# Performance work log

Measured on AMD Instinct MI355X. Metric: run time of the kernel, lower is better.

Reference implementation:

```python
import jax, jax.numpy as jnp
import numpy as np

# ---- static configuration (mirrors EarthSpecificBlock/EarthAttention3D) ----
WS = (2, 6, 12)                 # window_size (Z, H, W)
DIM = 192
HEADS = 6
DEPTH = 2
B, Z, H, W = 1, 8, 91, 180      # token grid entering the layer
PAD_H = (WS[1] - H % WS[1]) % WS[1]   # 5
PAD_W = (WS[2] - W % WS[2]) % WS[2]   # 0
HP, WP = H + PAD_H, W + PAD_W         # 96, 180
TOK = WS[0] * WS[1] * WS[2]           # 144 tokens per window
NZ, NH, NW = Z // WS[0], HP // WS[1], WP // WS[2]   # 4, 16, 15
TYPE_W = NZ * NH                      # 64 window types (Z x lat)
BIAS_ROWS = (2 * WS[2] - 1) * WS[1] * WS[1] * WS[0] * WS[0]  # 3312


def _construct_index():
    """Position index into the earth-specific bias table (EarthAttention3D._construct_index)."""
    zi = np.arange(WS[0]); zj = -np.arange(WS[0]) * WS[0]
    hi = np.arange(WS[1]); hj = -np.arange(WS[1]) * WS[1]
    w = np.arange(WS[2])
    c1 = np.stack(np.meshgrid(zi, hi, w, indexing='ij')).reshape(3, -1)
    c2 = np.stack(np.meshgrid(zj, hj, w, indexing='ij')).reshape(3, -1)
    coords = (c1[:, :, None] - c2[:, None, :]).transpose(1, 2, 0)
    coords[:, :, 2] += WS[2] - 1
    coords[:, :, 1] *= 2 * WS[2] - 1
    coords[:, :, 0] *= (2 * WS[2] - 1) * WS[1] * WS[1]
    return coords.sum(-1).reshape(-1)   # (TOK*TOK,)


def _gen_mask():
    """Shifted-window attention mask (gen_mask), shape (1, NW, TYPE_W, 1, TOK, TOK)."""
    m = np.zeros((1, Z, HP, WP, 1), np.float32)
    zs = (slice(0, -WS[0]), slice(-WS[0], -WS[0] // 2), slice(-WS[0] // 2, None))
    hs = (slice(0, -WS[1]), slice(-WS[1], -WS[1] // 2), slice(-WS[1] // 2, None))
    cnt = 0
    for zsl in zs:
        for hsl in hs:
            m[:, zsl, hsl, :, :] = cnt
            cnt += 1
    mw = m.reshape(1, NZ, WS[0], NH, WS[1], NW, WS[2], 1).transpose(0, 1, 3, 5, 2, 4, 6, 7)
    mw = mw.reshape(1, NZ, NH, NW, TOK)
    am = mw[:, :, :, :, None, :] - mw[:, :, :, :, :, None]
    am = np.where(am != 0, np.float32(-100.0), np.float32(0.0))
    return am.transpose(0, 3, 1, 2, 4, 5).reshape(1, NW, TYPE_W, 1, TOK, TOK)


POS_IDX = jnp.asarray(_construct_index())
MASK = jnp.asarray(_gen_mask())


def _ln(x, g, b):
    m = x.mean(-1, keepdims=True)
    v = ((x - m) ** 2).mean(-1, keepdims=True)
    return (x - m) * jax.lax.rsqrt(v + 1e-5) * g + b


def _block(x, qkv_w, qkv_b, proj_w, proj_b, bias_tab, g1, b1, g2, b2, w1, bm1, w2, bm2, roll):
    shortcut = x
    x = jnp.pad(x, ((0, 0), (0, 0), (0, PAD_H), (0, PAD_W), (0, 0)))
    if roll:
        x = jnp.roll(x, (-(WS[0] // 2), -(WS[1] // 2), -(WS[2] // 2)), axis=(1, 2, 3))
    # window partition: (B, NW, TYPE_W, TOK, C)
    xw = x.reshape(B, NZ, WS[0], NH, WS[1], NW, WS[2], DIM).transpose(0, 5, 1, 3, 2, 4, 6, 7)
    xw = xw.reshape(B, NW, TYPE_W, TOK, DIM)
    dh = DIM // HEADS
    qkv = (xw @ qkv_w + qkv_b).reshape(B, NW, TYPE_W, TOK, 3, HEADS, dh)
    qkv = qkv.transpose(4, 0, 1, 2, 5, 3, 6)   # (3, B, NW, TYPE_W, HEADS, TOK, dh)
    q, k, v = qkv[0], qkv[1], qkv[2]
    q = q * (dh ** -0.5)
    attn = jnp.einsum('bwphid,bwphjd->bwphij', q, k)
    bias = bias_tab[POS_IDX].reshape(TOK, TOK, TYPE_W, HEADS).transpose(2, 3, 0, 1)
    attn = attn + bias
    if roll:
        attn = attn + MASK
    attn = jax.nn.softmax(attn, axis=-1)
    out = jnp.einsum('bwphij,bwphjd->bwphid', attn, v)
    out = out.transpose(0, 1, 2, 4, 3, 5).reshape(B, NW, TYPE_W, TOK, DIM)
    out = out @ proj_w + proj_b
    # window merge back to (B, Z, HP, WP, C)
    x = out.reshape(B, NW, NZ, NH, WS[0], WS[1], WS[2], DIM).transpose(0, 2, 4, 3, 5, 1, 6, 7)
    x = x.reshape(B, Z, HP, WP, DIM)
    if roll:
        x = jnp.roll(x, (WS[0] // 2, WS[1] // 2, WS[2] // 2), axis=(1, 2, 3))
    x = x[:, :, :H, :W]
    x = shortcut + _ln(x, g1, b1)           # post-norm residual, as in source
    h = jax.nn.gelu(x @ w1 + bm1, approximate=False)
    h = h @ w2 + bm2
    return x + _ln(h, g2, b2)


def setup_inputs() -> dict:
    key = jax.random.key(0)
    ks = jax.random.split(key, 8)
    s = 0.02
    return {
        'x': jax.random.normal(ks[0], (B, Z, H, W, DIM), jnp.float32),
        'qkv_w': jax.random.normal(ks[1], (DEPTH, DIM, 3 * DIM), jnp.float32) * s,
        'qkv_b': jnp.zeros((DEPTH, 3 * DIM), jnp.float32),
        'proj_w': jax.random.normal(ks[2], (DEPTH, DIM, DIM), jnp.float32) * s,
        'proj_b': jnp.zeros((DEPTH, DIM), jnp.float32),
        'bias_tab': jax.random.normal(ks[3], (DEPTH, BIAS_ROWS, TYPE_W, HEADS), jnp.float32) * s,
        'norm1_g': jnp.ones((DEPTH, DIM), jnp.float32),
        'norm1_b': jnp.zeros((DEPTH, DIM), jnp.float32),
        'norm2_g': jnp.ones((DEPTH, DIM), jnp.float32),
        'norm2_b': jnp.zeros((DEPTH, DIM), jnp.float32),
        'mlp_w1': jax.random.normal(ks[4], (DEPTH, DIM, 4 * DIM), jnp.float32) * s,
        'mlp_b1': jnp.zeros((DEPTH, 4 * DIM), jnp.float32),
        'mlp_w2': jax.random.normal(ks[5], (DEPTH, 4 * DIM, DIM), jnp.float32) * s,
        'mlp_b2': jnp.zeros((DEPTH, DIM), jnp.float32),
    }


def reference(x, qkv_w, qkv_b, proj_w, proj_b, bias_tab, norm1_g, norm1_b,
              norm2_g, norm2_b, mlp_w1, mlp_b1, mlp_w2, mlp_b2):
    for i in range(DEPTH):
        x = _block(x, qkv_w[i], qkv_b[i], proj_w[i], proj_b[i], bias_tab[i],
                   norm1_g[i], norm1_b[i], norm2_g[i], norm2_b[i],
                   mlp_w1[i], mlp_b1[i], mlp_w2[i], mlp_b2[i], roll=(i % 2 == 1))
    return x
```

## Files before the change

kernel.cpp:

```cpp
#include <hip/hip_runtime.h>
#include <math.h>

#define NTOK   131040
#define NTOKW  138240

typedef __attribute__((ext_vector_type(8))) short bf16x8;
typedef __attribute__((ext_vector_type(8))) unsigned short u16x8;
typedef __attribute__((ext_vector_type(4))) float f32x4;
typedef __attribute__((ext_vector_type(2))) float f32x2;

__device__ __forceinline__ float b2f(unsigned short u){
  union { unsigned u; float f; } v; v.u = ((unsigned)u) << 16; return v.f;
}
__device__ __forceinline__ unsigned short f2b(float f){
  union { float f; unsigned u; } v; v.f = f;
  unsigned r = v.u + 0x7FFFu + ((v.u >> 16) & 1u);
  return (unsigned short)(r >> 16);
}
__device__ __forceinline__ float gelu_fast(float x){
  float t = 0.79788456080286536f * (x + 0.044715f * x * x * x);
  float e = __expf(2.0f * t);
  float th = 1.0f - 2.0f * __builtin_amdgcn_rcpf(e + 1.0f);
  return 0.5f * x * (1.0f + th);
}
__device__ __forceinline__ unsigned pk_bf16(float lo, float hi){
  unsigned r;
  asm("v_cvt_pk_bf16_f32 %0, %1, %2" : "=v"(r) : "v"(lo), "v"(hi));
  return r;
}
__device__ __forceinline__ void lds_barrier(){
  asm volatile("s_waitcnt lgkmcnt(0)" ::: "memory");
  __builtin_amdgcn_sched_barrier(0);
  __builtin_amdgcn_s_barrier();
  __builtin_amdgcn_sched_barrier(0);
}

__global__ __launch_bounds__(256) void transp(const float* __restrict__ src,
                                              unsigned short* __restrict__ dst,
                                              int K, int N){
  int i = blockIdx.x*256 + threadIdx.x;
  if (i < K*N){
    int n = i / K, k = i % K;
    dst[i] = f2b(src[(size_t)k*N + n]);
  }
}

__global__ __launch_bounds__(256) void bias_pre(
    const float* __restrict__ btab,
    unsigned short* __restrict__ bw,
    int roll)
{
  int gid = blockIdx.x*256 + threadIdx.x;
  int pair = gid / 20736;
  int rem  = gid % 20736;
  int i = rem / 144, j = rem % 144;
  int tw = pair / 6, head = pair % 6;
  int ia = i/72, ib = (i%72)/12, ic = i%12;
  int ja = j/72, jb = (j%72)/12, jc = j%12;
  int idx = (ia + 2*ja)*828 + (ib + 6*jb)*23 + (ic - jc + 11);
  float v = btab[(size_t)idx*384 + tw*6 + head];
  if (roll){
    int nz = tw >> 4, nh = tw & 15;
    int zi = nz*2+ia, hi = nh*6+ib, zj = nz*2+ja, hj = nh*6+jb;
    int ri = 3*((zi<6)?0:((zi<7)?1:2)) + ((hi<90)?0:((hi<93)?1:2));
    int rj = 3*((zj<6)?0:((zj<7)?1:2)) + ((hj<90)?0:((hj<93)?1:2));
    if (ri != rj) v -= 100.0f;
  }
  bw[gid] = f2b(v);
}

__global__ __launch_bounds__(256) void gather_win(const float* __restrict__ x,
                                                  unsigned short* __restrict__ xw,
                                                  int roll){
  int gid = blockIdx.x*256 + threadIdx.x;
  int row = gid / 24;
  int dp  = gid % 24;
  int tok = row % 144;
  int wt  = row / 144;
  int tw  = wt & 63;
  int w   = wt >> 6;
  int nz = tw >> 4, nh = tw & 15;
  int wz = tok / 72; int rem = tok % 72; int wh = rem / 12; int ww = rem % 12;
  int z = nz*2 + wz, h = nh*6 + wh, wc = w*12 + ww;
  if (roll){ z = (z+1)&7; h = (h+3)%96; wc = (wc+6)%180; }
  int d0 = dp*8;
  u16x8 o;
  if (h < 91){
    const float* s = x + ((size_t)((z*91 + h)*180 + wc))*192 + d0;
    #pragma unroll
    for (int i=0;i<8;i++) o[i] = f2b(s[i]);
  } else {
    #pragma unroll
    for (int i=0;i<8;i++) o[i] = 0;
  }
  *(u16x8*)(xw + (size_t)row*192 + d0) = o;
}

__global__ __launch_bounds__(512) void gemm_k192(
    const unsigned short* __restrict__ A,
    const unsigned short* __restrict__ Bt,
    const float* __restrict__ bias,
    unsigned short* __restrict__ C,
    int N)
{
  __shared__ unsigned short Bst[192][200];
  int m0 = blockIdx.x * 128;
  int n0 = blockIdx.y * 192;
  int t = threadIdx.x;
  int lane = t & 63, w = t >> 6;
  int wm = w >> 2, wn = w & 3;
  int lg = lane >> 4, lr = lane & 15;

  #pragma unroll
  for (int i=0;i<9;i++){
    int idx = t + i*512;
    int r = idx / 24, c = (idx % 24)*8;
    *(u16x8*)&Bst[r][c] = *(const u16x8*)(Bt + (size_t)(n0 + r)*192 + c);
  }
  __syncthreads();

  const unsigned short* aRow = A + (size_t)(m0 + wm*64 + lr)*192 + lg*8;

  f32x4 acc[4][3];
  #pragma unroll
  for (int a=0;a<4;a++)
    #pragma unroll
    for (int b=0;b<3;b++) acc[a][b] = (f32x4){0.f,0.f,0.f,0.f};

  bf16x8 aP[2][6];
  #pragma unroll
  for (int ks=0; ks<6; ks++) aP[0][ks] = *(const bf16x8*)(aRow + ks*32);

  #pragma unroll
  for (int rt=0; rt<4; rt++){
    if (rt < 3){
      const unsigned short* an = aRow + (size_t)(rt+1)*16*192;
      #pragma unroll
      for (int ks=0; ks<6; ks++) aP[(rt+1)&1][ks] = *(const bf16x8*)(an + ks*32);
    }
    #pragma unroll
    for (int ks=0; ks<6; ks++){
      bf16x8 b0 = *(const bf16x8*)&Bst[wn*48 +      lr][ks*32 + lg*8];
      bf16x8 b1 = *(const bf16x8*)&Bst[wn*48 + 16 + lr][ks*32 + lg*8];
      bf16x8 b2 = *(const bf16x8*)&Bst[wn*48 + 32 + lr][ks*32 + lg*8];
      bf16x8 af = aP[rt&1][ks];
      acc[rt][0] = __builtin_amdgcn_mfma_f32_16x16x32_bf16(af, b0, acc[rt][0], 0,0,0);
      acc[rt][1] = __builtin_amdgcn_mfma_f32_16x16x32_bf16(af, b1, acc[rt][1], 0,0,0);
      acc[rt][2] = __builtin_amdgcn_mfma_f32_16x16x32_bf16(af, b2, acc[rt][2], 0,0,0);
    }
  }

  #pragma unroll
  for (int rt=0; rt<4; rt++){
    #pragma unroll
    for (int fn=0; fn<3; fn++){
      int colg = n0 + wn*48 + fn*16 + lr;
      float bv = bias[colg];
      #pragma unroll
      for (int r=0;r<4;r++){
        int rowg = m0 + wm*64 + rt*16 + lg*4 + r;
        C[(size_t)rowg*N + colg] = f2b(acc[rt][fn][r] + bv);
      }
    }
  }
}

__global__ __launch_bounds__(576) void attn_win(
    const unsigned short* __restrict__ qkv,
    const unsigned short* __restrict__ bw,
    unsigned short* __restrict__ outp)
{
  __shared__ union {
    struct { unsigned short Qs[144][32]; unsigned short Ks[144][40]; } qk;
    unsigned short Ps[144][160];
  } U;
  __shared__ unsigned short Vst[32][160];

  int b = blockIdx.x;
  int head = b % 6;
  int wt = b / 6;
  int tw = wt & 63;
  int t = threadIdx.x;
  int lane = t & 63;
  int wv = t >> 6;
  int lg = lane >> 4, lr = lane & 15;

  {
    int tok = t >> 2, c0 = (t & 3)*8;
    size_t base = ((size_t)wt*144 + tok)*576 + head*32 + c0;
    u16x8 qv = *(const u16x8*)(qkv + base);
    u16x8 kv = *(const u16x8*)(qkv + base + 192);
    u16x8 vv = *(const u16x8*)(qkv + base + 384);
    u16x8 qs;
    #pragma unroll
    for (int i=0;i<8;i++) qs[i] = f2b(b2f(qv[i]) * 0.17677669529663687f);
    *(u16x8*)&U.qk.Qs[tok][c0] = qs;
    *(u16x8*)&U.qk.Ks[tok][c0] = kv;
    #pragma unroll
    for (int i=0;i<8;i++) Vst[c0+i][tok] = vv[i];
  }
  if (t < 512) Vst[t >> 4][144 + (t & 15)] = 0;
  __syncthreads();

  float s[9][4];
  {
    bf16x8 a = *(const bf16x8*)&U.qk.Qs[wv*16 + lr][lg*8];
    #pragma unroll
    for (int ct=0; ct<9; ct++){
      bf16x8 bb = *(const bf16x8*)&U.qk.Ks[ct*16 + lr][lg*8];
      f32x4 d = {0.f,0.f,0.f,0.f};
      d = __builtin_amdgcn_mfma_f32_16x16x32_bf16(a, bb, d, 0,0,0);
      s[ct][0]=d[0]; s[ct][1]=d[1]; s[ct][2]=d[2]; s[ct][3]=d[3];
    }
  }

  {
    const unsigned short* bp = bw + (size_t)(tw*6 + head)*20736;
    int i0 = wv*16 + lg*4;
    #pragma unroll
    for (int ct=0; ct<9; ct++){
      int j = ct*16 + lr;
      #pragma unroll
      for (int r=0;r<4;r++)
        s[ct][r] += b2f(bp[(i0 + r)*144 + j]);
    }
  }

  float mx[4] = {-1e30f,-1e30f,-1e30f,-1e30f};
  #pragma unroll
  for (int ct=0; ct<9; ct++)
    #pragma unroll
    for (int r=0;r<4;r++) mx[r] = fmaxf(mx[r], s[ct][r]);
  #pragma unroll
  for (int off=1; off<16; off<<=1)
    #pragma unroll
    for (int r=0;r<4;r++) mx[r] = fmaxf(mx[r], __shfl_xor(mx[r], off));
  float sm[4] = {0.f,0.f,0.f,0.f};
  #pragma unroll
  for (int ct=0; ct<9; ct++)
    #pragma unroll
    for (int r=0;r<4;r++){ s[ct][r] = __expf(s[ct][r] - mx[r]); sm[r] += s[ct][r]; }
  #pragma unroll
  for (int off=1; off<16; off<<=1)
    #pragma unroll
    for (int r=0;r<4;r++) sm[r] += __shfl_xor(sm[r], off);
  float inv[4];
  #pragma unroll
  for (int r=0;r<4;r++) inv[r] = 1.0f / sm[r];

  lds_barrier();

  #pragma unroll
  for (int ct=0; ct<9; ct++)
    #pragma unroll
    for (int r=0;r<4;r++)
      U.Ps[wv*16 + lg*4 + r][ct*16 + lr] = f2b(s[ct][r] * inv[r]);
  #pragma unroll
  for (int r=0;r<4;r++) U.Ps[wv*16 + lg*4 + r][144 + lr] = 0;
  __syncthreads();

  #pragma unroll
  for (int ct2=0; ct2<2; ct2++){
    f32x4 o = {0.f,0.f,0.f,0.f};
    #pragma unroll
    for (int kt=0; kt<5; kt++){
      bf16x8 a  = *(const bf16x8*)&U.Ps[wv*16 + lr][kt*32 + lg*8];
      bf16x8 bb = *(const bf16x8*)&Vst[ct2*16 + lr][kt*32 + lg*8];
      o = __builtin_amdgcn_mfma_f32_16x16x32_bf16(a, bb, o, 0,0,0);
    }
    size_t rb = ((size_t)wt*144 + wv*16 + lg*4)*192 + head*32 + ct2*16 + lr;
    #pragma unroll
    for (int r=0;r<4;r++) outp[rb + (size_t)r*192] = f2b(o[r]);
  }
}

__global__ __launch_bounds__(256) void unwin_ln(
  const unsigned short* __restrict__ ywin,
  const float* __restrict__ xsrc,
  const float* __restrict__ g, const float* __restrict__ bb,
  float* __restrict__ outf, unsigned short* __restrict__ outb, int roll)
{
  int tok = blockIdx.x*4 + (threadIdx.x>>6);
  if (tok >= NTOK) return;
  int lane = threadIdx.x & 63;
  int z = tok / (91*180);
  int rem = tok % (91*180);
  int h = rem / 180, wc = rem % 180;
  int zz=z, hh=h, ww=wc;
  if (roll){ zz = (z+7)&7; hh = (h+93)%96; ww = (wc+174)%180; }
  int nz = zz>>1, wz = zz&1;
  int nh = hh/6,  wh = hh%6;
  int nw = ww/12, w2 = ww%12;
  size_t row = ((size_t)(nw*64 + nz*16 + nh))*144 + wz*72 + wh*12 + w2;
  const unsigned short* yr = ywin + row*192;
  float v[3]; float s=0.f, ss=0.f;
  #pragma unroll
  for (int i=0;i<3;i++){ v[i] = b2f(yr[lane + i*64]); s += v[i]; ss += v[i]*v[i]; }
  #pragma unroll
  for (int off=32; off>=1; off>>=1){ s += __shfl_xor(s, off); ss += __shfl_xor(ss, off); }
  float mean = s * (1.0f/192.0f);
  float var = ss * (1.0f/192.0f) - mean*mean;
  float rinv = rsqrtf(var + 1e-5f);
  size_t tb = (size_t)tok*192;
  #pragma unroll
  for (int i=0;i<3;i++){
    int d = lane + i*64;
    float o = xsrc[tb + d] + ((v[i]-mean)*rinv*g[d] + bb[d]);
    outf[tb+d] = o;
    outb[tb+d] = f2b(o);
  }
}

__global__ __launch_bounds__(512) void mlp_fused_ln(
    const unsigned short* __restrict__ A,
    const unsigned short* __restrict__ W1t,
    const float* __restrict__ bias1,
    const unsigned short* __restrict__ W2t,
    const float* __restrict__ mbias2,
    const float* __restrict__ xmid,
    const float* __restrict__ lng,
    const float* __restrict__ lnb,
    float* __restrict__ outF,
    int M)
{
  __shared__ unsigned short W1s[2][32][196];
  __shared__ unsigned short W2s[2][192][44];
  __shared__ unsigned short Hs[8][32][40];
  __shared__ float b1s[768];
  __shared__ float eps[576];
  int m0 = blockIdx.x*256;
  int t = threadIdx.x, lane = t & 63, w = t >> 6;
  int lg = lane >> 4, lr = lane & 15;

  bf16x8 afrA[6], afrB[6];
  {
    int ra = m0 + w*32 + lr, rb = ra + 16;
    if (ra < M){
      const unsigned short* ap = A + (size_t)ra*192 + lg*8;
      #pragma unroll
      for (int ks=0; ks<6; ks++) afrA[ks] = *(const bf16x8*)(ap + ks*32);
    } else {
      #pragma unroll
      for (int ks=0; ks<6; ks++)
        #pragma unroll
        for (int j=0;j<8;j++) afrA[ks][j] = 0;
    }
    if (rb < M){
      const unsigned short* ap = A + (size_t)rb*192 + lg*8;
      #pragma unroll
      for (int ks=0; ks<6; ks++) afrB[ks] = *(const bf16x8*)(ap + ks*32);
    } else {
      #pragma unroll
      for (int ks=0; ks<6; ks++)
        #pragma unroll
        for (int j=0;j<8;j++) afrB[ks][j] = 0;
    }
  }

  b1s[t] = bias1[t];
  if (t < 256) b1s[512 + t] = bias1[512 + t];
  if (t < 192){ eps[t] = mbias2[t]; eps[192 + t] = lng[t]; eps[384 + t] = lnb[t]; }

  int i1r[2], i1c[2], i2r[2], i2c[2];
  #pragma unroll
  for (int i=0;i<2;i++){
    int idx = t + i*512;
    i1r[i] = idx/24; i1c[i] = (idx%24)*8;
    i2r[i] = idx/4;  i2c[i] = (idx&3)*8;
  }
  bool g2nd = (t + 512) < 768;

  {
    u16x8 a0 = *(const u16x8*)(W1t + (size_t)i1r[0]*192 + i1c[0]);
    u16x8 b0 = *(const u16x8*)(W2t + (size_t)i2r[0]*768 + i2c[0]);
    *(u16x8*)&W1s[0][i1r[0]][i1c[0]] = a0;
    *(u16x8*)&W2s[0][i2r[0]][i2c[0]] = b0;
    if (g2nd){
      u16x8 a1 = *(const u16x8*)(W1t + (size_t)i1r[1]*192 + i1c[1]);
      u16x8 b1v = *(const u16x8*)(W2t + (size_t)i2r[1]*768 + i2c[1]);
      *(u16x8*)&W1s[0][i1r[1]][i1c[1]] = a1;
      *(u16x8*)&W2s[0][i2r[1]][i2c[1]] = b1v;
    }
  }
  lds_barrier();

  f32x4 accA[12], accB[12];
  #pragma unroll
  for (int i=0;i<12;i++){ accA[i] = (f32x4){0.f,0.f,0.f,0.f}; accB[i] = (f32x4){0.f,0.f,0.f,0.f}; }

  u16x8 w1r[2], w2r[2];

  for (int it=0; it<24; ++it){
    int cur = it & 1;
    if (it < 23){
      int hc2 = (it+1)*32;
      w1r[0] = *(const u16x8*)(W1t + (size_t)(hc2 + i1r[0])*192 + i1c[0]);
      w2r[0] = *(const u16x8*)(W2t + (size_t)i2r[0]*768 + hc2 + i2c[0]);
      if (g2nd){
        w1r[1] = *(const u16x8*)(W1t + (size_t)(hc2 + i1r[1])*192 + i1c[1]);
        w2r[1] = *(const u16x8*)(W2t + (size_t)i2r[1]*768 + hc2 + i2c[1]);
      }
    }

    int hc = it*32;
    f32x4 h0a = (f32x4){0.f,0.f,0.f,0.f}, h1a = h0a, h0b = h0a, h1b = h0a;
    #pragma unroll
    for (int ks=0; ks<6; ks++){
      bf16x8 b0  = *(const bf16x8*)&W1s[cur][2*lr    ][ks*32 + lg*8];
      bf16x8 b1f = *(const bf16x8*)&W1s[cur][2*lr + 1][ks*32 + lg*8];
      h0a = __builtin_amdgcn_mfma_f32_16x16x32_bf16(afrA[ks], b0,  h0a, 0,0,0);
      h1a = __builtin_amdgcn_mfma_f32_16x16x32_bf16(afrA[ks], b1f, h1a, 0,0,0);
      h0b = __builtin_amdgcn_mfma_f32_16x16x32_bf16(afrB[ks], b0,  h0b, 0,0,0);
      h1b = __builtin_amdgcn_mfma_f32_16x16x32_bf16(afrB[ks], b1f, h1b, 0,0,0);
    }
    float bb0 = b1s[hc + 2*lr];
    float bb1 = b1s[hc + 2*lr + 1];
    #pragma unroll
    for (int r=0;r<4;r++){
      *(unsigned*)&Hs[w][lg*4 + r][2*lr] =
          pk_bf16(gelu_fast(h0a[r] + bb0), gelu_fast(h1a[r] + bb1));
      *(unsigned*)&Hs[w][16 + lg*4 + r][2*lr] =
          pk_bf16(gelu_fast(h0b[r] + bb0), gelu_fast(h1b[r] + bb1));
    }
    bf16x8 paA = *(const bf16x8*)&Hs[w][lr][lg*8];
    bf16x8 paB = *(const bf16x8*)&Hs[w][16 + lr][lg*8];
    #pragma unroll
    for (int f=0; f<6; f++){
      bf16x8 c0 = *(const bf16x8*)&W2s[cur][f*32 + 2*lr    ][lg*8];
      bf16x8 c1 = *(const bf16x8*)&W2s[cur][f*32 + 2*lr + 1][lg*8];
      accA[2*f]   = __builtin_amdgcn_mfma_f32_16x16x32_bf16(paA, c0, accA[2*f],   0,0,0);
      accA[2*f+1] = __builtin_amdgcn_mfma_f32_16x16x32_bf16(paA, c1, accA[2*f+1], 0,0,0);
      accB[2*f]   = __builtin_amdgcn_mfma_f32_16x16x32_bf16(paB, c0, accB[2*f],   0,0,0);
      accB[2*f+1] = __builtin_amdgcn_mfma_f32_16x16x32_bf16(paB, c1, accB[2*f+1], 0,0,0);
    }

    if (it < 23){
      int nxt = cur ^ 1;
      *(u16x8*)&W1s[nxt][i1r[0]][i1c[0]] = w1r[0];
      *(u16x8*)&W2s[nxt][i2r[0]][i2c[0]] = w2r[0];
      if (g2nd){
        *(u16x8*)&W1s[nxt][i1r[1]][i1c[1]] = w1r[1];
        *(u16x8*)&W2s[nxt][i2r[1]][i2c[1]] = w2r[1];
      }
    }
    lds_barrier();
  }

  #pragma unroll
  for (int gsel=0; gsel<2; gsel++){
    f32x4* acc = gsel ? accB : accA;
    #pragma unroll
    for (int r=0;r<4;r++){
      int row = m0 + w*32 + gsel*16 + lg*4 + r;
      float s = 0.f, ss = 0.f;
      #pragma unroll
      for (int f=0; f<6; f++){
        float v0 = acc[2*f][r]   + eps[f*32 + 2*lr];
        float v1 = acc[2*f+1][r] + eps[f*32 + 2*lr + 1];
        s += v0 + v1; ss += v0*v0 + v1*v1;
      }
      #pragma unroll
      for (int off=1; off<16; off<<=1){ s += __shfl_xor(s, off); ss += __shfl_xor(ss, off); }
      float mean = s * (1.0f/192.0f);
      float var  = ss * (1.0f/192.0f) - mean*mean;
      float rinv = rsqrtf(var + 1e-5f);
      if (row < M){
        size_t base = (size_t)row*192;
        #pragma unroll
        for (int f=0; f<6; f++){
          int c0 = f*32 + 2*lr;
          float v0 = acc[2*f][r]   + eps[c0];
          float v1 = acc[2*f+1][r] + eps[c0 + 1];
          f32x2 xm = *(const f32x2*)&xmid[base + c0];
          f32x2 o;
          o[0] = xm[0] + (v0 - mean)*rinv*eps[192 + c0]     + eps[384 + c0];
          o[1] = xm[1] + (v1 - mean)*rinv*eps[192 + c0 + 1] + eps[384 + c0 + 1];
          *(f32x2*)&outF[base + c0] = o;
        }
      }
    }
  }
}

extern "C" void kernel_launch(void* const* d_in, const int* in_sizes, int n_in,
                              void* d_out, int out_size, void* d_ws, size_t ws_size,
                              hipStream_t stream)
{
  const float* x_in    = (const float*)d_in[0];
  const float* qkvw    = (const float*)d_in[1];
  const float* qkvbias = (const float*)d_in[2];
  const float* projw   = (const float*)d_in[3];
  const float* projbias= (const float*)d_in[4];
  const float* btab    = (const float*)d_in[5];
  const float* n1g = (const float*)d_in[6];
  const float* n1b = (const float*)d_in[7];
  const float* n2g = (const float*)d_in[8];
  const float* n2b = (const float*)d_in[9];
  const float* w1  = (const float*)d_in[10];
  const float* b1  = (const float*)d_in[11];
  const float* w2  = (const float*)d_in[12];
  const float* b2  = (const float*)d_in[13];
  float* outp = (float*)d_out;

  const size_t REG_A = (size_t)NTOKW*192;
  const size_t REG_B = (size_t)NTOKW*576;
  const size_t W_QT  = (size_t)2*576*192;
  const size_t W_PT  = (size_t)2*192*192;
  const size_t W_1T  = (size_t)2*768*192;
  const size_t W_2T  = (size_t)2*192*768;
  const size_t TOT_SH = REG_A + REG_B + W_QT + W_PT + W_1T + W_2T;
  const size_t NEEDED = TOT_SH*2 + (size_t)NTOK*192*4;
  if (ws_size < NEEDED) return;

  unsigned short* ws16 = (unsigned short*)d_ws;
  size_t off = 0;
  unsigned short* regA = ws16 + off; off += REG_A;
  unsigned short* regB = ws16 + off; off += REG_B;
  unsigned short* wqt  = ws16 + off; off += W_QT;
  unsigned short* wpt  = ws16 + off; off += W_PT;
  unsigned short* w1t  = ws16 + off; off += W_1T;
  unsigned short* w2t  = ws16 + off; off += W_2T;
  float* xmidf = (float*)(ws16 + off);
  unsigned short* bw = (unsigned short*)xmidf;

  for (int dep=0; dep<2; dep++){
    transp<<<(192*576+255)/256,256,0,stream>>>(qkvw + (size_t)dep*192*576,
                                               wqt + (size_t)dep*576*192, 192, 576);
    transp<<<(192*192+255)/256,256,0,stream>>>(projw + (size_t)dep*192*192,
                                               wpt + (size_t)dep*192*192, 192, 192);
    transp<<<(192*768+255)/256,256,0,stream>>>(w1 + (size_t)dep*192*768,
                                               w1t + (size_t)dep*768*192, 192, 768);
    transp<<<(768*192+255)/256,256,0,stream>>>(w2 + (size_t)dep*768*192,
                                               w2t + (size_t)dep*192*768, 768, 192);
  }

  for (int dep=0; dep<2; dep++){
    int roll = dep;
    const float* xs = (dep==0) ? x_in : outp;
    float* xout = outp;

    gather_win<<<NTOKW*24/256, 256, 0, stream>>>(xs, regA, roll);

    dim3 g1(NTOKW/128, 3);
    gemm_k192<<<g1, 512, 0, stream>>>(regA, wqt + (size_t)dep*576*192,
                                      qkvbias + dep*576, regB, 576);

    bias_pre<<<(64*6*20736)/256, 256, 0, stream>>>(btab + (size_t)dep*3312*384, bw, roll);

    attn_win<<<960*6, 576, 0, stream>>>(regB, bw, regA);

    dim3 g2(NTOKW/128, 1);
    gemm_k192<<<g2, 512, 0, stream>>>(regA, wpt + (size_t)dep*192*192,
                                      projbias + dep*192, regB, 192);

    unwin_ln<<<NTOK/4, 256, 0, stream>>>(regB, xs, n1g + dep*192, n1b + dep*192,
                                         xmidf, regA, roll);

    mlp_fused_ln<<<(NTOK+255)/256, 512, 0, stream>>>(
        regA, w1t + (size_t)dep*768*192, b1 + dep*768,
        w2t + (size_t)dep*192*768, b2 + dep*192,
        xmidf, n2g + dep*192, n2b + dep*192, xout, NTOK);
  }
}
```

Before: 1.081 ms.

## Fuse projection GEMM with unwindow+LayerNorm and prelayout attention bias per lane

```diff
diff --git a/kernel.cpp b/kernel.cpp
--- a/kernel.cpp
+++ b/kernel.cpp
@@ -51,22 +51,34 @@
     int roll)
 {
   int gid = blockIdx.x*256 + threadIdx.x;
-  int pair = gid / 20736;
-  int rem  = gid % 20736;
-  int i = rem / 144, j = rem % 144;
-  int tw = pair / 6, head = pair % 6;
-  int ia = i/72, ib = (i%72)/12, ic = i%12;
-  int ja = j/72, jb = (j%72)/12, jc = j%12;
-  int idx = (ia + 2*ja)*828 + (ib + 6*jb)*23 + (ic - jc + 11);
-  float v = btab[(size_t)idx*384 + tw*6 + head];
-  if (roll){
-    int nz = tw >> 4, nh = tw & 15;
-    int zi = nz*2+ia, hi = nh*6+ib, zj = nz*2+ja, hj = nh*6+jb;
-    int ri = 3*((zi<6)?0:((zi<7)?1:2)) + ((hi<90)?0:((hi<93)?1:2));
-    int rj = 3*((zj<6)?0:((zj<7)?1:2)) + ((hj<90)?0:((hj<93)?1:2));
-    if (ri != rj) v -= 100.0f;
-  }
-  bw[gid] = f2b(v);
+  int e    = gid % 40;
+  int rem  = gid / 40;
+  int lane = rem % 64;
+  int rem2 = rem / 64;
+  int wv   = rem2 % 9;
+  int slice= rem2 / 9;
+  unsigned short out = 0;
+  if (e < 36){
+    int ct = e >> 2, r = e & 3;
+    int i = wv*16 + (lane>>4)*4 + r;
+    int j = ct*16 + (lane & 15);
+    int tw = slice / 6, head = slice % 6;
+    int ia = i/72, ib = (i%72)/12, ic = i%12;
+    int ja = j/72, jb = (j%72)/12, jc = j%12;
+    int idx = (ia + 2*ja)*828 + (ib + 6*jb)*23 + (ic - jc + 11);
+    float v = btab[(size_t)idx*384 + tw*6 + head];
+    if (roll){
+      int nz = tw >> 4, nh = tw & 15;
+      int zi = nz*2+ia, hi = nh*6+ib, zj = nz*2+ja, hj = nh*6+jb;
+      int ri = 3*((zi<6)?0:((zi<7)?1:2)) + ((hi<90)?0:((hi<93)?1:2));
+      int rj = 3*((zj<6)?0:((zj<7)?1:2)) + ((hj<90)?0:((hj<93)?1:2));
+      if (ri != rj) v -= 100.0f;
+    }
+    out = f2b(v);
+  }
+  int vec = e >> 3, elem = e & 7;
+  size_t di = ((((size_t)slice*9 + wv)*5 + vec)*64 + lane)*8 + elem;
+  bw[di] = out;
 }
 
 __global__ __launch_bounds__(256) void gather_win(const float* __restrict__ x,
@@ -165,6 +177,138 @@
   }
 }
 
+__global__ __launch_bounds__(512) void proj_ln(
+    const unsigned short* __restrict__ A,
+    const unsigned short* __restrict__ Bt,
+    const float* __restrict__ bias,
+    const float* __restrict__ xsrc,
+    const float* __restrict__ g,
+    const float* __restrict__ bb,
+    float* __restrict__ outf,
+    unsigned short* __restrict__ outb,
+    int roll)
+{
+  __shared__ unsigned short Bst[192][200];
+  __shared__ float Psum[128][4];
+  __shared__ float Psq [128][4];
+  int m0 = blockIdx.x * 128;
+  int t = threadIdx.x;
+  int lane = t & 63, w = t >> 6;
+  int wm = w >> 2, wn = w & 3;
+  int lg = lane >> 4, lr = lane & 15;
+
+  #pragma unroll
+  for (int i=0;i<9;i++){
+    int idx = t + i*512;
+    int r = idx / 24, c = (idx % 24)*8;
+    *(u16x8*)&Bst[r][c] = *(const u16x8*)(Bt + (size_t)r*192 + c);
+  }
+  __syncthreads();
+
+  const unsigned short* aRow = A + (size_t)(m0 + wm*64 + lr)*192 + lg*8;
+
+  f32x4 acc[4][3];
+  #pragma unroll
+  for (int a=0;a<4;a++)
+    #pragma unroll
+    for (int b=0;b<3;b++) acc[a][b] = (f32x4){0.f,0.f,0.f,0.f};
+
+  bf16x8 aP[2][6];
+  #pragma unroll
+  for (int ks=0; ks<6; ks++) aP[0][ks] = *(const bf16x8*)(aRow + ks*32);
+
+  #pragma unroll
+  for (int rt=0; rt<4; rt++){
+    if (rt < 3){
+      const unsigned short* an = aRow + (size_t)(rt+1)*16*192;
+      #pragma unroll
+      for (int ks=0; ks<6; ks++) aP[(rt+1)&1][ks] = *(const bf16x8*)(an + ks*32);
+    }
+    #pragma unroll
+    for (int ks=0; ks<6; ks++){
+      bf16x8 b0 = *(const bf16x8*)&Bst[wn*48 +      lr][ks*32 + lg*8];
+      bf16x8 b1 = *(const bf16x8*)&Bst[wn*48 + 16 + lr][ks*32 + lg*8];
+      bf16x8 b2 = *(const bf16x8*)&Bst[wn*48 + 32 + lr][ks*32 + lg*8];
+      bf16x8 af = aP[rt&1][ks];
+      acc[rt][0] = __builtin_amdgcn_mfma_f32_16x16x32_bf16(af, b0, acc[rt][0], 0,0,0);
+      acc[rt][1] = __builtin_amdgcn_mfma_f32_16x16x32_bf16(af, b1, acc[rt][1], 0,0,0);
+      acc[rt][2] = __builtin_amdgcn_mfma_f32_16x16x32_bf16(af, b2, acc[rt][2], 0,0,0);
+    }
+  }
+
+  float bv[3];
+  #pragma unroll
+  for (int fn=0; fn<3; fn++) bv[fn] = bias[wn*48 + fn*16 + lr];
+
+  float sp[4][4], sq[4][4];
+  #pragma unroll
+  for (int rt=0; rt<4; rt++){
+    #pragma unroll
+    for (int r=0;r<4;r++){
+      float s = 0.f, ss = 0.f;
+      #pragma unroll
+      for (int fn=0; fn<3; fn++){
+        float v = acc[rt][fn][r] + bv[fn];
+        acc[rt][fn][r] = v;
+        s += v; ss += v*v;
+      }
+      #pragma unroll
+      for (int off=1; off<16; off<<=1){
+        s  += __shfl_xor(s,  off);
+        ss += __shfl_xor(ss, off);
+      }
+      sp[rt][r] = s; sq[rt][r] = ss;
+    }
+  }
+  if (lr == 0){
+    #pragma unroll
+    for (int rt=0; rt<4; rt++)
+      #pragma unroll
+      for (int r=0;r<4;r++){
+        int row = wm*64 + rt*16 + lg*4 + r;
+        Psum[row][wn] = sp[rt][r];
+        Psq [row][wn] = sq[rt][r];
+      }
+  }
+  lds_barrier();
+
+  #pragma unroll
+  for (int rt=0; rt<4; rt++){
+    #pragma unroll
+    for (int r=0;r<4;r++){
+      int row = wm*64 + rt*16 + lg*4 + r;
+      f32x4 s4 = *(const f32x4*)&Psum[row][0];
+      f32x4 q4 = *(const f32x4*)&Psq [row][0];
+      float s  = s4[0]+s4[1]+s4[2]+s4[3];
+      float ss = q4[0]+q4[1]+q4[2]+q4[3];
+      float mean = s * (1.0f/192.0f);
+      float var  = ss * (1.0f/192.0f) - mean*mean;
+      float rinv = rsqrtf(var + 1e-5f);
+
+      int grow = m0 + row;
+      int wt = grow / 144, tok = grow % 144;
+      int tw = wt & 63, wwi = wt >> 6;
+      int nz = tw >> 4, nh = tw & 15;
+      int wz = tok / 72; int trem = tok % 72; int wh = trem / 12; int wwp = trem % 12;
+      int zz = nz*2 + wz, hh = nh*6 + wh, ww2 = wwi*12 + wwp;
+      int z, h, wc;
+      if (roll){ z = (zz+1)&7; h = (hh+3)%96; wc = (ww2+6)%180; }
+      else     { z = zz; h = hh; wc = ww2; }
+      if (h < 91){
+        size_t tb = ((size_t)(z*91 + h)*180 + wc)*192;
+        #pragma unroll
+        for (int fn=0; fn<3; fn++){
+          int col = wn*48 + fn*16 + lr;
+          float v = acc[rt][fn][r];
+          float o = xsrc[tb + col] + (v - mean)*rinv*g[col] + bb[col];
+          outf[tb + col] = o;
+          outb[tb + col] = f2b(o);
+        }
+      }
+    }
+  }
+}
+
 __global__ __launch_bounds__(576) void attn_win(
     const unsigned short* __restrict__ qkv,
     const unsigned short* __restrict__ bw,
@@ -200,6 +344,16 @@
     for (int i=0;i<8;i++) Vst[c0+i][tok] = vv[i];
   }
   if (t < 512) Vst[t >> 4][144 + (t & 15)] = 0;
+
+  u16x8 bv0, bv1, bv2, bv3, bv4;
+  {
+    size_t sbase = ((((size_t)(tw*6 + head))*9 + wv)*5*64 + lane)*8;
+    bv0 = *(const u16x8*)(bw + sbase);
+    bv1 = *(const u16x8*)(bw + sbase + 64*8);
+    bv2 = *(const u16x8*)(bw + sbase + 2*64*8);
+    bv3 = *(const u16x8*)(bw + sbase + 3*64*8);
+    bv4 = *(const u16x8*)(bw + sbase + 4*64*8);
+  }
   __syncthreads();
 
   float s[9][4];
@@ -214,15 +368,17 @@
     }
   }
 
-  {
-    const unsigned short* bp = bw + (size_t)(tw*6 + head)*20736;
-    int i0 = wv*16 + lg*4;
-    #pragma unroll
-    for (int ct=0; ct<9; ct++){
-      int j = ct*16 + lr;
-      #pragma unroll
-      for (int r=0;r<4;r++)
-        s[ct][r] += b2f(bp[(i0 + r)*144 + j]);
+  #pragma unroll
+  for (int ct=0; ct<9; ct++){
+    #pragma unroll
+    for (int r=0;r<4;r++){
+      const int e = ct*4 + r;
+      unsigned short bu =
+        (e < 8)  ? bv0[e & 7] :
+        (e < 16) ? bv1[e & 7] :
+        (e < 24) ? bv2[e & 7] :
+        (e < 32) ? bv3[e & 7] : bv4[e & 7];
+      s[ct][r] += b2f(bu);
     }
   }
 
@@ -271,43 +427,6 @@
     size_t rb = ((size_t)wt*144 + wv*16 + lg*4)*192 + head*32 + ct2*16 + lr;
     #pragma unroll
     for (int r=0;r<4;r++) outp[rb + (size_t)r*192] = f2b(o[r]);
-  }
-}
-
-__global__ __launch_bounds__(256) void unwin_ln(
-  const unsigned short* __restrict__ ywin,
-  const float* __restrict__ xsrc,
-  const float* __restrict__ g, const float* __restrict__ bb,
-  float* __restrict__ outf, unsigned short* __restrict__ outb, int roll)
-{
-  int tok = blockIdx.x*4 + (threadIdx.x>>6);
-  if (tok >= NTOK) return;
-  int lane = threadIdx.x & 63;
-  int z = tok / (91*180);
-  int rem = tok % (91*180);
-  int h = rem / 180, wc = rem % 180;
-  int zz=z, hh=h, ww=wc;
-  if (roll){ zz = (z+7)&7; hh = (h+93)%96; ww = (wc+174)%180; }
-  int nz = zz>>1, wz = zz&1;
-  int nh = hh/6,  wh = hh%6;
-  int nw = ww/12, w2 = ww%12;
-  size_t row = ((size_t)(nw*64 + nz*16 + nh))*144 + wz*72 + wh*12 + w2;
-  const unsigned short* yr = ywin + row*192;
-  float v[3]; float s=0.f, ss=0.f;
-  #pragma unroll
-  for (int i=0;i<3;i++){ v[i] = b2f(yr[lane + i*64]); s += v[i]; ss += v[i]*v[i]; }
-  #pragma unroll
-  for (int off=32; off>=1; off>>=1){ s += __shfl_xor(s, off); ss += __shfl_xor(ss, off); }
-  float mean = s * (1.0f/192.0f);
-  float var = ss * (1.0f/192.0f) - mean*mean;
-  float rinv = rsqrtf(var + 1e-5f);
-  size_t tb = (size_t)tok*192;
-  #pragma unroll
-  for (int i=0;i<3;i++){
-    int d = lane + i*64;
-    float o = xsrc[tb + d] + ((v[i]-mean)*rinv*g[d] + bb[d]);
-    outf[tb+d] = o;
-    outb[tb+d] = f2b(o);
   }
 }
 
@@ -545,19 +664,17 @@
     gemm_k192<<<g1, 512, 0, stream>>>(regA, wqt + (size_t)dep*576*192,
                                       qkvbias + dep*576, regB, 576);
 
-    bias_pre<<<(64*6*20736)/256, 256, 0, stream>>>(btab + (size_t)dep*3312*384, bw, roll);
+    bias_pre<<<(384*9*64*40)/256, 256, 0, stream>>>(btab + (size_t)dep*3312*384, bw, roll);
 
     attn_win<<<960*6, 576, 0, stream>>>(regB, bw, regA);
 
-    dim3 g2(NTOKW/128, 1);
-    gemm_k192<<<g2, 512, 0, stream>>>(regA, wpt + (size_t)dep*192*192,
-                                      projbias + dep*192, regB, 192);
-
-    unwin_ln<<<NTOK/4, 256, 0, stream>>>(regB, xs, n1g + dep*192, n1b + dep*192,
-                                         xmidf, regA, roll);
+    proj_ln<<<NTOKW/128, 512, 0, stream>>>(regA, wpt + (size_t)dep*192*192,
+                                           projbias + dep*192, xs,
+                                           n1g + dep*192, n1b + dep*192,
+                                           xmidf, regB, roll);
 
     mlp_fused_ln<<<(NTOK+255)/256, 512, 0, stream>>>(
-        regA, w1t + (size_t)dep*768*192, b1 + dep*768,
+        regB, w1t + (size_t)dep*768*192, b1 + dep*768,
         w2t + (size_t)dep*192*768, b2 + dep*192,
         xmidf, n2g + dep*192, n2b + dep*192, xout, NTOK);
   }
```

Result: slower. 1.132 ms (+4.7%).

## Store attention bias in MFMA fragment order and prefetch it before the barrier

Applied to the files above, without the earlier changes.

```diff
diff --git a/kernel.cpp b/kernel.cpp
--- a/kernel.cpp
+++ b/kernel.cpp
@@ -51,22 +51,38 @@
     int roll)
 {
   int gid = blockIdx.x*256 + threadIdx.x;
-  int pair = gid / 20736;
-  int rem  = gid % 20736;
-  int i = rem / 144, j = rem % 144;
-  int tw = pair / 6, head = pair % 6;
-  int ia = i/72, ib = (i%72)/12, ic = i%12;
-  int ja = j/72, jb = (j%72)/12, jc = j%12;
-  int idx = (ia + 2*ja)*828 + (ib + 6*jb)*23 + (ic - jc + 11);
-  float v = btab[(size_t)idx*384 + tw*6 + head];
-  if (roll){
-    int nz = tw >> 4, nh = tw & 15;
-    int zi = nz*2+ia, hi = nh*6+ib, zj = nz*2+ja, hj = nh*6+jb;
-    int ri = 3*((zi<6)?0:((zi<7)?1:2)) + ((hi<90)?0:((hi<93)?1:2));
-    int rj = 3*((zj<6)?0:((zj<7)?1:2)) + ((hj<90)?0:((hj<93)?1:2));
-    if (ri != rj) v -= 100.0f;
-  }
-  bw[gid] = f2b(v);
+  int lane = gid & 63;
+  int rem  = gid >> 6;
+  int vec  = rem % 5;
+  int rem2 = rem / 5;
+  int wv   = rem2 % 9;
+  int slice= rem2 / 9;
+  int tw = slice / 6, head = slice % 6;
+  int nz = tw >> 4, nh = tw & 15;
+  u16x8 out;
+  #pragma unroll
+  for (int elem=0; elem<8; elem++){
+    int e = vec*8 + elem;
+    unsigned short o = 0;
+    if (e < 36){
+      int ct = e >> 2, r = e & 3;
+      int i = wv*16 + (lane>>4)*4 + r;
+      int j = ct*16 + (lane & 15);
+      int ia = i/72, ib = (i%72)/12, ic = i%12;
+      int ja = j/72, jb = (j%72)/12, jc = j%12;
+      int idx = (ia + 2*ja)*828 + (ib + 6*jb)*23 + (ic - jc + 11);
+      float v = btab[(size_t)idx*384 + slice];
+      if (roll){
+        int zi = nz*2+ia, hi = nh*6+ib, zj = nz*2+ja, hj = nh*6+jb;
+        int ri = 3*((zi<6)?0:((zi<7)?1:2)) + ((hi<90)?0:((hi<93)?1:2));
+        int rj = 3*((zj<6)?0:((zj<7)?1:2)) + ((hj<90)?0:((hj<93)?1:2));
+        if (ri != rj) v -= 100.0f;
+      }
+      o = f2b(v);
+    }
+    out[elem] = o;
+  }
+  *(u16x8*)(bw + (size_t)gid*8) = out;
 }
 
 __global__ __launch_bounds__(256) void gather_win(const float* __restrict__ x,
@@ -200,6 +216,16 @@
     for (int i=0;i<8;i++) Vst[c0+i][tok] = vv[i];
   }
   if (t < 512) Vst[t >> 4][144 + (t & 15)] = 0;
+
+  u16x8 bv0, bv1, bv2, bv3, bv4;
+  {
+    size_t sbase = ((((size_t)(tw*6 + head))*9 + wv)*5*64 + lane)*8;
+    bv0 = *(const u16x8*)(bw + sbase);
+    bv1 = *(const u16x8*)(bw + sbase + 64*8);
+    bv2 = *(const u16x8*)(bw + sbase + 2*64*8);
+    bv3 = *(const u16x8*)(bw + sbase + 3*64*8);
+    bv4 = *(const u16x8*)(bw + sbase + 4*64*8);
+  }
   __syncthreads();
 
   float s[9][4];
@@ -214,15 +240,17 @@
     }
   }
 
-  {
-    const unsigned short* bp = bw + (size_t)(tw*6 + head)*20736;
-    int i0 = wv*16 + lg*4;
-    #pragma unroll
-    for (int ct=0; ct<9; ct++){
-      int j = ct*16 + lr;
-      #pragma unroll
-      for (int r=0;r<4;r++)
-        s[ct][r] += b2f(bp[(i0 + r)*144 + j]);
+  #pragma unroll
+  for (int ct=0; ct<9; ct++){
+    #pragma unroll
+    for (int r=0;r<4;r++){
+      const int e = ct*4 + r;
+      unsigned short bu =
+        (e < 8)  ? bv0[e & 7] :
+        (e < 16) ? bv1[e & 7] :
+        (e < 24) ? bv2[e & 7] :
+        (e < 32) ? bv3[e & 7] : bv4[e & 7];
+      s[ct][r] += b2f(bu);
     }
   }
 
@@ -545,7 +573,7 @@
     gemm_k192<<<g1, 512, 0, stream>>>(regA, wqt + (size_t)dep*576*192,
                                       qkvbias + dep*576, regB, 576);
 
-    bias_pre<<<(64*6*20736)/256, 256, 0, stream>>>(btab + (size_t)dep*3312*384, bw, roll);
+    bias_pre<<<(384*9*5*64)/256, 256, 0, stream>>>(btab + (size_t)dep*3312*384, bw, roll);
 
     attn_win<<<960*6, 576, 0, stream>>>(regB, bw, regA);
 
```

Result: faster. 1.051 ms (-2.7%).
